# Kernel tuning notes

Hardware: AMD Instinct MI355X
Metric: run time of the kernel (lower is better)

Reference implementation:

```python
import jax, jax.numpy as jnp
import numpy as np

B, T, C = 2, 2048, 2048
N_HEADS, HEAD_DIM = 16, 128
THETA = 10000.0


def _rope_cos_sin(T, dim, theta=THETA):
    inv_freq = 1.0 / (theta ** (jnp.arange(0, dim, 2, dtype=jnp.float32) / dim))  # (dim/2,)
    t = jnp.arange(T, dtype=jnp.float32)
    freqs = jnp.outer(t, inv_freq)  # (T, dim/2)
    return jnp.cos(freqs), jnp.sin(freqs)


def _apply_rope(x, cos, sin):
    # x: (B, H, T, D); cos/sin: (T, D/2) -> broadcast over B, H
    xr = x[..., 0::2]
    xi = x[..., 1::2]
    or_ = xr * cos - xi * sin
    oi_ = xr * sin + xi * cos
    return jnp.stack([or_, oi_], axis=-1).reshape(x.shape)


def setup_inputs() -> dict:
    key = jax.random.key(0)
    ks = jax.random.split(key, 5)
    scale = 1.0 / np.sqrt(C)
    x = jax.random.normal(ks[0], (B, T, C), dtype=jnp.float32)
    wq = jax.random.normal(ks[1], (C, N_HEADS * HEAD_DIM), dtype=jnp.float32) * scale
    wk = jax.random.normal(ks[2], (C, N_HEADS * HEAD_DIM), dtype=jnp.float32) * scale
    wv = jax.random.normal(ks[3], (C, N_HEADS * HEAD_DIM), dtype=jnp.float32) * scale
    wo = jax.random.normal(ks[4], (N_HEADS * HEAD_DIM, C), dtype=jnp.float32) * scale
    mask = jnp.tril(jnp.ones((T, T), dtype=bool))[None, None]  # causal (1,1,T,T)
    return {"x": x, "mask": mask, "wq": wq, "wk": wk, "wv": wv, "wo": wo}


def reference(x, mask, wq, wk, wv, wo):
    Bx, Tx, Cx = x.shape
    cos, sin = _rope_cos_sin(Tx, HEAD_DIM)
    # projections -> (B, H, T, D)
    def proj(w):
        return (x @ w).reshape(Bx, Tx, N_HEADS, HEAD_DIM).transpose(0, 2, 1, 3)
    q = _apply_rope(proj(wq), cos, sin)
    k = _apply_rope(proj(wk), cos, sin)
    v = proj(wv)
    scores = jnp.einsum("bhqd,bhkd->bhqk", q, k) / jnp.sqrt(jnp.float32(HEAD_DIM))
    scores = jnp.where(mask, scores, -jnp.inf)
    attn = jax.nn.softmax(scores, axis=-1)
    out = jnp.einsum("bhqk,bhkd->bhqd", attn, v)
    out = out.transpose(0, 2, 1, 3).reshape(Bx, Tx, Cx)
    return out @ wo
```

## Files before the change

kernel.cpp:

```cpp
#include <hip/hip_runtime.h>
#include <stdint.h>

#define B_  2
#define T_  2048
#define C_  2048
#define NH  16
#define HD  128
#define M_  (B_*T_)

typedef unsigned short ushort_t;
typedef unsigned int uint;
typedef __attribute__((ext_vector_type(8))) short short8;
typedef __attribute__((ext_vector_type(4))) float f32x4;
typedef __attribute__((ext_vector_type(16))) float f32x16;

#if __has_builtin(__builtin_amdgcn_exp2f)
#define EXP2 __builtin_amdgcn_exp2f
#else
#define EXP2 exp2f
#endif

__device__ inline ushort_t f2b(float f) {
  union { float f; unsigned u; } x; x.f = f;
  unsigned r = (x.u + 0x7fffu + ((x.u >> 16) & 1u)) >> 16;
  return (ushort_t)r;
}
__device__ inline float b2f(ushort_t b) {
  union { unsigned u; float f; } x; x.u = ((unsigned)b) << 16;
  return x.f;
}
__device__ inline uint cvtpk(float lo, float hi) {
  uint d;
  asm("v_cvt_pk_bf16_f32 %0, %1, %2" : "=v"(d) : "v"(lo), "v"(hi));
  return d;
}
__device__ inline void pl32swap(uint& a, uint& b) {
  asm volatile("v_permlane32_swap_b32 %0, %1" : "+v"(a), "+v"(b));
}
__device__ inline void gload_lds16(const void* g, void* l) {
  __builtin_amdgcn_global_load_lds((const __attribute__((address_space(1))) void*)g,
                                   (__attribute__((address_space(3))) void*)l, 16, 0, 0);
}

__global__ __launch_bounds__(256) void cvt_f32_bf16(const float* __restrict__ in,
                                                    ushort_t* __restrict__ out, int n4) {
  int i = blockIdx.x * 256 + threadIdx.x;
  if (i >= n4) return;
  float4 v = ((const float4*)in)[i];
  unsigned long long pk = (unsigned long long)f2b(v.x)
                        | ((unsigned long long)f2b(v.y) << 16)
                        | ((unsigned long long)f2b(v.z) << 32)
                        | ((unsigned long long)f2b(v.w) << 48);
  ((unsigned long long*)out)[i] = pk;
}

template<int FROM_F32>
__global__ __launch_bounds__(256) void transpose_to_bf16(const void* __restrict__ inv,
                                                         ushort_t* __restrict__ out,
                                                         int rows, int cols) {
  __shared__ __align__(16) ushort_t tile[64][72];
  const int t = threadIdx.x;
  const int br = blockIdx.y * 64, bc = blockIdx.x * 64;
  if (FROM_F32) {
    const float* in = (const float*)inv;
    const int vc = t & 15, r0 = t >> 4;
#pragma unroll
    for (int i = 0; i < 4; i++) {
      int row = r0 + 16 * i;
      float4 v = *(const float4*)&in[(size_t)(br + row) * cols + bc + vc * 4];
      tile[row][vc * 4 + 0] = f2b(v.x);
      tile[row][vc * 4 + 1] = f2b(v.y);
      tile[row][vc * 4 + 2] = f2b(v.z);
      tile[row][vc * 4 + 3] = f2b(v.w);
    }
  } else {
    const ushort_t* in = (const ushort_t*)inv;
    const int vc = t & 7, r0 = t >> 3;
#pragma unroll
    for (int i = 0; i < 2; i++) {
      int row = r0 + 32 * i;
      short8 v = *(const short8*)&in[(size_t)(br + row) * cols + bc + vc * 8];
#pragma unroll
      for (int j = 0; j < 8; j++) tile[row][vc * 8 + j] = (ushort_t)v[j];
    }
  }
  __syncthreads();
  const int oc = t >> 2;
#pragma unroll
  for (int s2 = 0; s2 < 2; s2++) {
    int seg = (t & 3) + 4 * s2;
    short8 w;
#pragma unroll
    for (int j = 0; j < 8; j++) w[j] = (short)tile[seg * 8 + j][oc];
    *(short8*)&out[(size_t)(bc + oc) * rows + br + seg * 8] = w;
  }
}

__global__ __launch_bounds__(256) void rope_table(float* __restrict__ cs, float* __restrict__ sn) {
  int i = blockIdx.x * 256 + threadIdx.x;
  int tt = i >> 6, f = i & 63;
  float inv = powf(10000.0f, -(float)(2 * f) / 128.0f);
  float ang = (float)tt * inv;
  cs[i] = cosf(ang);
  sn[i] = sinf(ang);
}

__global__ __launch_bounds__(256) void rope_apply(ushort_t* __restrict__ Q, ushort_t* __restrict__ K,
                                                  const float* __restrict__ cs,
                                                  const float* __restrict__ sn) {
  int i = blockIdx.x * 256 + threadIdx.x;
  int row = i >> 8, g = i & 255;
  int tt = row & (T_ - 1);
  int fb = (g * 4) & 63;
  f32x4 cv = *(const f32x4*)&cs[(tt << 6) + fb];
  f32x4 sv = *(const f32x4*)&sn[(tt << 6) + fb];
  size_t idx = ((size_t)row << 11) + (size_t)g * 8;
  short8 q = *(const short8*)&Q[idx];
  short8 k = *(const short8*)&K[idx];
#pragma unroll
  for (int j = 0; j < 4; j++) {
    float c = cv[j], s = sv[j];
    float qr = b2f((ushort_t)q[2 * j]), qi = b2f((ushort_t)q[2 * j + 1]);
    q[2 * j]     = (short)f2b(qr * c - qi * s);
    q[2 * j + 1] = (short)f2b(qr * s + qi * c);
    float kr = b2f((ushort_t)k[2 * j]), ki = b2f((ushort_t)k[2 * j + 1]);
    k[2 * j]     = (short)f2b(kr * c - ki * s);
    k[2 * j + 1] = (short)f2b(kr * s + ki * c);
  }
  *(short8*)&Q[idx] = q;
  *(short8*)&K[idx] = k;
}

template<int OUTF32>
__global__ __launch_bounds__(512, 2) void gemm_bt3(const ushort_t* __restrict__ A,
                                                   const ushort_t* __restrict__ Bt0,
                                                   const ushort_t* __restrict__ Bt1,
                                                   const ushort_t* __restrict__ Bt2,
                                                   void* __restrict__ O0, void* __restrict__ O1,
                                                   void* __restrict__ O2, int N, int K) {
  extern __shared__ __align__(16) ushort_t lds[];
  const int z = blockIdx.z;
  const ushort_t* Bt = (z == 0) ? Bt0 : (z == 1) ? Bt1 : Bt2;
  void* Ov = (z == 0) ? O0 : (z == 1) ? O1 : O2;
  const int tid = threadIdx.x;
  const int lane = tid & 63, wave = tid >> 6;
  const int lr = lane & 15, lg = lane >> 4;
  const int wm = wave >> 1, wn = wave & 1;
  const int swz = lr & 7;
  const int bm = blockIdx.y, bn = blockIdx.x;
  const ushort_t* Ap = A + (size_t)bm * 256 * K;
  const ushort_t* Bp = Bt + (size_t)bn * 128 * K;
  const int NT = K >> 6;

  f32x4 acc[4][4] = {};

  auto stage = [&](int k0, int buf) {
    const int base = buf * 24576;
#pragma unroll
    for (int i = 0; i < 4; i++) {
      int idx = i * 512 + tid;
      int row = idx >> 3;
      int c = (idx & 7) ^ (row & 7);
      gload_lds16(Ap + (size_t)row * K + k0 + c * 8, &lds[(size_t)(base + idx * 8)]);
    }
#pragma unroll
    for (int i = 0; i < 2; i++) {
      int idx = i * 512 + tid;
      int row = idx >> 3;
      int c = (idx & 7) ^ (row & 7);
      gload_lds16(Bp + (size_t)row * K + k0 + c * 8, &lds[(size_t)(base + 16384 + idx * 8)]);
    }
  };

  stage(0, 0);
  stage(64, 1);

  for (int t = 0; t < NT; t++) {
    if (t + 2 < NT) stage((t + 2) << 6, (t + 2) % 3);
    if (t < NT - 2)       asm volatile("s_waitcnt vmcnt(12)" ::: "memory");
    else if (t == NT - 2) asm volatile("s_waitcnt vmcnt(6)"  ::: "memory");
    else                  asm volatile("s_waitcnt vmcnt(0)"  ::: "memory");
    __builtin_amdgcn_s_barrier();
    const int abase = (t % 3) * 24576, bbase = abase + 16384;
    __builtin_amdgcn_s_setprio(1);
#pragma unroll
    for (int kk = 0; kk < 2; kk++) {
      short8 af[4], bf[4];
      const int ch = ((kk * 4 + lg) ^ swz) * 8;
#pragma unroll
      for (int mf = 0; mf < 4; mf++)
        af[mf] = *(const short8*)&lds[abase + (wm * 64 + mf * 16 + lr) * 64 + ch];
#pragma unroll
      for (int nf = 0; nf < 4; nf++)
        bf[nf] = *(const short8*)&lds[bbase + (wn * 64 + nf * 16 + lr) * 64 + ch];
#pragma unroll
      for (int mf = 0; mf < 4; mf++)
#pragma unroll
        for (int nf = 0; nf < 4; nf++)
          acc[mf][nf] = __builtin_amdgcn_mfma_f32_16x16x32_bf16(af[mf], bf[nf], acc[mf][nf], 0, 0, 0);
    }
    __builtin_amdgcn_s_setprio(0);
    __builtin_amdgcn_s_barrier();
  }

  const int row0 = bm * 256 + wm * 64 + lg * 4;
  const int col0 = bn * 128 + wn * 64 + lr;
  if (OUTF32) {
    float* O = (float*)Ov;
#pragma unroll
    for (int mf = 0; mf < 4; mf++)
#pragma unroll
      for (int nf = 0; nf < 4; nf++)
#pragma unroll
        for (int r = 0; r < 4; r++)
          O[(size_t)(row0 + mf * 16 + r) * N + col0 + nf * 16] = acc[mf][nf][r];
  } else {
    ushort_t* O = (ushort_t*)Ov;
#pragma unroll
    for (int mf = 0; mf < 4; mf++)
#pragma unroll
      for (int nf = 0; nf < 4; nf++)
#pragma unroll
        for (int r = 0; r < 4; r++)
          O[(size_t)(row0 + mf * 16 + r) * N + col0 + nf * 16] = f2b(acc[mf][nf][r]);
  }
}

__global__ __launch_bounds__(64) void flash_attn3(const ushort_t* __restrict__ Q,
                                                  const ushort_t* __restrict__ K,
                                                  const ushort_t* __restrict__ Vt,
                                                  ushort_t* __restrict__ AO) {
  int flat = blockIdx.x;
  int swz = (flat & 7) * 128 + (flat >> 3);
  const int bh = swz >> 5, widx = swz & 31;
  const int b = bh >> 4, h = bh & 15;
  const int lane = threadIdx.x & 63;
  const int col = lane & 31, hi = lane >> 5, hioff = 4 * hi;
  const ushort_t* Qb = Q + (size_t)b * T_ * C_ + (size_t)h * HD;
  const ushort_t* Kb = K + (size_t)b * T_ * C_ + (size_t)h * HD;
  const ushort_t* Vb = Vt + (size_t)bh * (size_t)HD * T_;
  const float sc = 0.12754245f;

#pragma unroll 1
  for (int ph = 0; ph < 2; ph++) {
    const int tile = ph ? (63 - widx) : widx;
    const int q0 = tile * 32;
    const int qcol = q0 + col;
    short8 qf[8];
#pragma unroll
    for (int db = 0; db < 8; db++)
      qf[db] = *(const short8*)&Qb[(size_t)qcol * C_ + db * 16 + hi * 8];

    f32x16 o0 = {}, o1 = {}, o2 = {}, o3 = {};
    float m = -1e30f, l = 0.f;

    short8 kf[8];
#pragma unroll
    for (int db = 0; db < 8; db++)
      kf[db] = *(const short8*)&Kb[(size_t)col * C_ + db * 16 + hi * 8];

#pragma unroll 1
    for (int k0 = 0; k0 <= q0; k0 += 32) {
      f32x16 s = {};
#pragma unroll
      for (int db = 0; db < 8; db++)
        s = __builtin_amdgcn_mfma_f32_32x32x16_bf16(kf[db], qf[db], s, 0, 0, 0);
      if (k0 + 32 <= q0) {
#pragma unroll
        for (int db = 0; db < 8; db++)
          kf[db] = *(const short8*)&Kb[(size_t)(k0 + 32 + col) * C_ + db * 16 + hi * 8];
      }
      short8 va[4][2];
#pragma unroll
      for (int dblk = 0; dblk < 4; dblk++)
#pragma unroll
        for (int j = 0; j < 2; j++)
          va[dblk][j] = *(const short8*)&Vb[(size_t)(dblk * 32 + col) * T_ + k0 + j * 16 + hi * 8];

      const bool domask = (k0 + 31 > q0);
      if (domask) {
#pragma unroll
        for (int r = 0; r < 16; r++) {
          int krow = k0 + ((r & 3) + 8 * (r >> 2)) + hioff;
          float v = s[r] * sc;
          s[r] = (krow > qcol) ? -1e30f : v;
        }
      } else {
#pragma unroll
        for (int r = 0; r < 16; r++) s[r] = s[r] * sc;
      }
      float tm = s[0];
#pragma unroll
      for (int r = 1; r < 16; r++) tm = fmaxf(tm, s[r]);
      tm = fmaxf(tm, __shfl_xor(tm, 32, 64));
      if (!__all(tm <= m + 8.0f)) {
        float mn = fmaxf(m, tm);
        float corr = EXP2(m - mn);
        m = mn;
        l *= corr;
#pragma unroll
        for (int r = 0; r < 16; r++) { o0[r] *= corr; o1[r] *= corr; o2[r] *= corr; o3[r] *= corr; }
      }
#pragma unroll
      for (int r = 0; r < 16; r++) s[r] = EXP2(s[r] - m);
      float rs = s[0];
#pragma unroll
      for (int r = 1; r < 16; r++) rs += s[r];
      rs += __shfl_xor(rs, 32, 64);
      l += rs;
      uint c0 = cvtpk(s[0], s[1]),  c1 = cvtpk(s[2], s[3]);
      uint c2 = cvtpk(s[4], s[5]),  c3 = cvtpk(s[6], s[7]);
      uint c4 = cvtpk(s[8], s[9]),  c5 = cvtpk(s[10], s[11]);
      uint c6 = cvtpk(s[12], s[13]), c7 = cvtpk(s[14], s[15]);
      pl32swap(c0, c2); pl32swap(c1, c3);
      pl32swap(c4, c6); pl32swap(c5, c7);
      union { uint u[4]; short8 v; } pb0, pb1;
      pb0.u[0] = c0; pb0.u[1] = c1; pb0.u[2] = c2; pb0.u[3] = c3;
      pb1.u[0] = c4; pb1.u[1] = c5; pb1.u[2] = c6; pb1.u[3] = c7;
      o0 = __builtin_amdgcn_mfma_f32_32x32x16_bf16(va[0][0], pb0.v, o0, 0, 0, 0);
      o1 = __builtin_amdgcn_mfma_f32_32x32x16_bf16(va[1][0], pb0.v, o1, 0, 0, 0);
      o2 = __builtin_amdgcn_mfma_f32_32x32x16_bf16(va[2][0], pb0.v, o2, 0, 0, 0);
      o3 = __builtin_amdgcn_mfma_f32_32x32x16_bf16(va[3][0], pb0.v, o3, 0, 0, 0);
      o0 = __builtin_amdgcn_mfma_f32_32x32x16_bf16(va[0][1], pb1.v, o0, 0, 0, 0);
      o1 = __builtin_amdgcn_mfma_f32_32x32x16_bf16(va[1][1], pb1.v, o1, 0, 0, 0);
      o2 = __builtin_amdgcn_mfma_f32_32x32x16_bf16(va[2][1], pb1.v, o2, 0, 0, 0);
      o3 = __builtin_amdgcn_mfma_f32_32x32x16_bf16(va[3][1], pb1.v, o3, 0, 0, 0);
    }
    float inv = 1.0f / l;
    size_t rowbase = (size_t)(b * T_ + qcol) * C_ + h * HD;
#pragma unroll
    for (int r = 0; r < 16; r++) {
      int d = (r & 3) + 8 * (r >> 2) + hioff;
      AO[rowbase + d]      = f2b(o0[r] * inv);
      AO[rowbase + 32 + d] = f2b(o1[r] * inv);
      AO[rowbase + 64 + d] = f2b(o2[r] * inv);
      AO[rowbase + 96 + d] = f2b(o3[r] * inv);
    }
  }
}

extern "C" void kernel_launch(void* const* d_in, const int* in_sizes, int n_in,
                              void* d_out, int out_size, void* d_ws, size_t ws_size,
                              hipStream_t stream) {
  const float* x  = (const float*)d_in[0];
  const float* wq = (const float*)d_in[2];
  const float* wk = (const float*)d_in[3];
  const float* wv = (const float*)d_in[4];
  const float* wo = (const float*)d_in[5];

  char* ws = (char*)d_ws;
  size_t off = 0;
  auto alloc = [&](size_t bytes) { char* p = ws + off; off += (bytes + 255) & ~255ull; return p; };
  ushort_t* Qb  = (ushort_t*)alloc((size_t)M_ * C_ * 2);
  ushort_t* Kb  = (ushort_t*)alloc((size_t)M_ * C_ * 2);
  ushort_t* Vb  = (ushort_t*)alloc((size_t)M_ * C_ * 2);
  ushort_t* Vtb = (ushort_t*)alloc((size_t)M_ * C_ * 2);
  ushort_t* xb  = (ushort_t*)alloc((size_t)M_ * C_ * 2);
  ushort_t* AO  = xb;
  ushort_t* wqt = (ushort_t*)alloc((size_t)C_ * C_ * 2);
  ushort_t* wkt = (ushort_t*)alloc((size_t)C_ * C_ * 2);
  ushort_t* wvt = (ushort_t*)alloc((size_t)C_ * C_ * 2);
  ushort_t* wot = (ushort_t*)alloc((size_t)C_ * C_ * 2);
  float* cs = (float*)alloc((size_t)T_ * 64 * 4);
  float* sn = (float*)alloc((size_t)T_ * 64 * 4);

  cvt_f32_bf16<<<(M_ * C_ / 4 + 255) / 256, 256, 0, stream>>>(x, xb, M_ * C_ / 4);
  dim3 tg(C_ / 64, C_ / 64);
  transpose_to_bf16<1><<<tg, 256, 0, stream>>>(wq, wqt, C_, C_);
  transpose_to_bf16<1><<<tg, 256, 0, stream>>>(wk, wkt, C_, C_);
  transpose_to_bf16<1><<<tg, 256, 0, stream>>>(wv, wvt, C_, C_);
  transpose_to_bf16<1><<<tg, 256, 0, stream>>>(wo, wot, C_, C_);
  rope_table<<<T_ * 64 / 256, 256, 0, stream>>>(cs, sn);
  gemm_bt3<0><<<dim3(C_ / 128, M_ / 256, 3), 512, 147456, stream>>>(
      xb, wqt, wkt, wvt, Qb, Kb, Vb, C_, C_);
  rope_apply<<<M_ * C_ / 8 / 256, 256, 0, stream>>>(Qb, Kb, cs, sn);
  for (int b = 0; b < B_; b++)
    transpose_to_bf16<0><<<dim3(T_ / 64, T_ / 64), 256, 0, stream>>>(
        Vb + (size_t)b * T_ * C_, Vtb + (size_t)b * T_ * C_, T_, C_);
  flash_attn3<<<dim3(B_ * NH * 32), 64, 0, stream>>>(Qb, Kb, Vtb, AO);
  gemm_bt3<1><<<dim3(C_ / 128, M_ / 256, 1), 512, 147456, stream>>>(
      AO, wot, wot, wot, d_out, d_out, d_out, C_, C_);
  (void)in_sizes; (void)n_in; (void)out_size; (void)ws_size;
}
```

Before: 456.7 us.

## Split causal KV loop across two waves per block with LDS merge

```diff
diff --git a/kernel.cpp b/kernel.cpp
--- a/kernel.cpp
+++ b/kernel.cpp
@@ -226,14 +226,17 @@
   }
 }
 
-__global__ __launch_bounds__(64) void flash_attn3(const ushort_t* __restrict__ Q,
-                                                  const ushort_t* __restrict__ K,
-                                                  const ushort_t* __restrict__ Vt,
-                                                  ushort_t* __restrict__ AO) {
+__global__ __launch_bounds__(128) void flash_attn4(const ushort_t* __restrict__ Q,
+                                                   const ushort_t* __restrict__ K,
+                                                   const ushort_t* __restrict__ Vt,
+                                                   ushort_t* __restrict__ AO) {
+  __shared__ float oLds[2][64][64];
+  __shared__ float mlLds[2][2][32];
   int flat = blockIdx.x;
   int swz = (flat & 7) * 128 + (flat >> 3);
   const int bh = swz >> 5, widx = swz & 31;
   const int b = bh >> 4, h = bh & 15;
+  const int w = threadIdx.x >> 6;
   const int lane = threadIdx.x & 63;
   const int col = lane & 31, hi = lane >> 5, hioff = 4 * hi;
   const ushort_t* Qb = Q + (size_t)b * T_ * C_ + (size_t)h * HD;
@@ -253,89 +256,109 @@
 
     f32x16 o0 = {}, o1 = {}, o2 = {}, o3 = {};
     float m = -1e30f, l = 0.f;
-
-    short8 kf[8];
-#pragma unroll
-    for (int db = 0; db < 8; db++)
-      kf[db] = *(const short8*)&Kb[(size_t)col * C_ + db * 16 + hi * 8];
+    const int kstart = w * 32;
+
+    if (kstart <= q0) {
+      short8 kf[8];
+#pragma unroll
+      for (int db = 0; db < 8; db++)
+        kf[db] = *(const short8*)&Kb[(size_t)(kstart + col) * C_ + db * 16 + hi * 8];
 
 #pragma unroll 1
-    for (int k0 = 0; k0 <= q0; k0 += 32) {
-      f32x16 s = {};
-#pragma unroll
-      for (int db = 0; db < 8; db++)
-        s = __builtin_amdgcn_mfma_f32_32x32x16_bf16(kf[db], qf[db], s, 0, 0, 0);
-      if (k0 + 32 <= q0) {
-#pragma unroll
-        for (int db = 0; db < 8; db++)
-          kf[db] = *(const short8*)&Kb[(size_t)(k0 + 32 + col) * C_ + db * 16 + hi * 8];
+      for (int k0 = kstart; k0 <= q0; k0 += 64) {
+        f32x16 sa = {}, sb = {};
+#pragma unroll
+        for (int db = 0; db < 4; db++) {
+          sa = __builtin_amdgcn_mfma_f32_32x32x16_bf16(kf[db],     qf[db],     sa, 0, 0, 0);
+          sb = __builtin_amdgcn_mfma_f32_32x32x16_bf16(kf[db + 4], qf[db + 4], sb, 0, 0, 0);
+        }
+        if (k0 + 64 <= q0) {
+#pragma unroll
+          for (int db = 0; db < 8; db++)
+            kf[db] = *(const short8*)&Kb[(size_t)(k0 + 64 + col) * C_ + db * 16 + hi * 8];
+        }
+        short8 va[4][2];
+#pragma unroll
+        for (int dblk = 0; dblk < 4; dblk++)
+#pragma unroll
+          for (int j = 0; j < 2; j++)
+            va[dblk][j] = *(const short8*)&Vb[(size_t)(dblk * 32 + col) * T_ + k0 + j * 16 + hi * 8];
+
+        f32x16 s;
+        const bool domask = (k0 + 31 > q0);
+        if (domask) {
+#pragma unroll
+          for (int r = 0; r < 16; r++) {
+            int krow = k0 + ((r & 3) + 8 * (r >> 2)) + hioff;
+            float v = (sa[r] + sb[r]) * sc;
+            s[r] = (krow > qcol) ? -1e30f : v;
+          }
+        } else {
+#pragma unroll
+          for (int r = 0; r < 16; r++) s[r] = (sa[r] + sb[r]) * sc;
+        }
+        float tm = s[0];
+#pragma unroll
+        for (int r = 1; r < 16; r++) tm = fmaxf(tm, s[r]);
+        tm = fmaxf(tm, __shfl_xor(tm, 32, 64));
+        if (!__all(tm <= m + 8.0f)) {
+          float mn = fmaxf(m, tm);
+          float corr = EXP2(m - mn);
+          m = mn;
+          l *= corr;
+#pragma unroll
+          for (int r = 0; r < 16; r++) { o0[r] *= corr; o1[r] *= corr; o2[r] *= corr; o3[r] *= corr; }
+        }
+#pragma unroll
+        for (int r = 0; r < 16; r++) s[r] = EXP2(s[r] - m);
+        float rs = s[0];
+#pragma unroll
+        for (int r = 1; r < 16; r++) rs += s[r];
+        rs += __shfl_xor(rs, 32, 64);
+        l += rs;
+        uint c0 = cvtpk(s[0], s[1]),  c1 = cvtpk(s[2], s[3]);
+        uint c2 = cvtpk(s[4], s[5]),  c3 = cvtpk(s[6], s[7]);
+        uint c4 = cvtpk(s[8], s[9]),  c5 = cvtpk(s[10], s[11]);
+        uint c6 = cvtpk(s[12], s[13]), c7 = cvtpk(s[14], s[15]);
+        pl32swap(c0, c2); pl32swap(c1, c3);
+        pl32swap(c4, c6); pl32swap(c5, c7);
+        union { uint u[4]; short8 v; } pb0, pb1;
+        pb0.u[0] = c0; pb0.u[1] = c1; pb0.u[2] = c2; pb0.u[3] = c3;
+        pb1.u[0] = c4; pb1.u[1] = c5; pb1.u[2] = c6; pb1.u[3] = c7;
+        o0 = __builtin_amdgcn_mfma_f32_32x32x16_bf16(va[0][0], pb0.v, o0, 0, 0, 0);
+        o1 = __builtin_amdgcn_mfma_f32_32x32x16_bf16(va[1][0], pb0.v, o1, 0, 0, 0);
+        o2 = __builtin_amdgcn_mfma_f32_32x32x16_bf16(va[2][0], pb0.v, o2, 0, 0, 0);
+        o3 = __builtin_amdgcn_mfma_f32_32x32x16_bf16(va[3][0], pb0.v, o3, 0, 0, 0);
+        o0 = __builtin_amdgcn_mfma_f32_32x32x16_bf16(va[0][1], pb1.v, o0, 0, 0, 0);
+        o1 = __builtin_amdgcn_mfma_f32_32x32x16_bf16(va[1][1], pb1.v, o1, 0, 0, 0);
+        o2 = __builtin_amdgcn_mfma_f32_32x32x16_bf16(va[2][1], pb1.v, o2, 0, 0, 0);
+        o3 = __builtin_amdgcn_mfma_f32_32x32x16_bf16(va[3][1], pb1.v, o3, 0, 0, 0);
       }
-      short8 va[4][2];
-#pragma unroll
-      for (int dblk = 0; dblk < 4; dblk++)
-#pragma unroll
-        for (int j = 0; j < 2; j++)
-          va[dblk][j] = *(const short8*)&Vb[(size_t)(dblk * 32 + col) * T_ + k0 + j * 16 + hi * 8];
-
-      const bool domask = (k0 + 31 > q0);
-      if (domask) {
-#pragma unroll
-        for (int r = 0; r < 16; r++) {
-          int krow = k0 + ((r & 3) + 8 * (r >> 2)) + hioff;
-          float v = s[r] * sc;
-          s[r] = (krow > qcol) ? -1e30f : v;
-        }
-      } else {
-#pragma unroll
-        for (int r = 0; r < 16; r++) s[r] = s[r] * sc;
-      }
-      float tm = s[0];
-#pragma unroll
-      for (int r = 1; r < 16; r++) tm = fmaxf(tm, s[r]);
-      tm = fmaxf(tm, __shfl_xor(tm, 32, 64));
-      if (!__all(tm <= m + 8.0f)) {
-        float mn = fmaxf(m, tm);
-        float corr = EXP2(m - mn);
-        m = mn;
-        l *= corr;
-#pragma unroll
-        for (int r = 0; r < 16; r++) { o0[r] *= corr; o1[r] *= corr; o2[r] *= corr; o3[r] *= corr; }
-      }
-#pragma unroll
-      for (int r = 0; r < 16; r++) s[r] = EXP2(s[r] - m);
-      float rs = s[0];
-#pragma unroll
-      for (int r = 1; r < 16; r++) rs += s[r];
-      rs += __shfl_xor(rs, 32, 64);
-      l += rs;
-      uint c0 = cvtpk(s[0], s[1]),  c1 = cvtpk(s[2], s[3]);
-      uint c2 = cvtpk(s[4], s[5]),  c3 = cvtpk(s[6], s[7]);
-      uint c4 = cvtpk(s[8], s[9]),  c5 = cvtpk(s[10], s[11]);
-      uint c6 = cvtpk(s[12], s[13]), c7 = cvtpk(s[14], s[15]);
-      pl32swap(c0, c2); pl32swap(c1, c3);
-      pl32swap(c4, c6); pl32swap(c5, c7);
-      union { uint u[4]; short8 v; } pb0, pb1;
-      pb0.u[0] = c0; pb0.u[1] = c1; pb0.u[2] = c2; pb0.u[3] = c3;
-      pb1.u[0] = c4; pb1.u[1] = c5; pb1.u[2] = c6; pb1.u[3] = c7;
-      o0 = __builtin_amdgcn_mfma_f32_32x32x16_bf16(va[0][0], pb0.v, o0, 0, 0, 0);
-      o1 = __builtin_amdgcn_mfma_f32_32x32x16_bf16(va[1][0], pb0.v, o1, 0, 0, 0);
-      o2 = __builtin_amdgcn_mfma_f32_32x32x16_bf16(va[2][0], pb0.v, o2, 0, 0, 0);
-      o3 = __builtin_amdgcn_mfma_f32_32x32x16_bf16(va[3][0], pb0.v, o3, 0, 0, 0);
-      o0 = __builtin_amdgcn_mfma_f32_32x32x16_bf16(va[0][1], pb1.v, o0, 0, 0, 0);
-      o1 = __builtin_amdgcn_mfma_f32_32x32x16_bf16(va[1][1], pb1.v, o1, 0, 0, 0);
-      o2 = __builtin_amdgcn_mfma_f32_32x32x16_bf16(va[2][1], pb1.v, o2, 0, 0, 0);
-      o3 = __builtin_amdgcn_mfma_f32_32x32x16_bf16(va[3][1], pb1.v, o3, 0, 0, 0);
-    }
-    float inv = 1.0f / l;
+    }
+#pragma unroll
+    for (int r = 0; r < 16; r++) {
+      oLds[w][r][lane]      = o0[r];
+      oLds[w][16 + r][lane] = o1[r];
+      oLds[w][32 + r][lane] = o2[r];
+      oLds[w][48 + r][lane] = o3[r];
+    }
+    if (lane < 32) { mlLds[w][0][lane] = m; mlLds[w][1][lane] = l; }
+    __syncthreads();
+    float m0 = mlLds[0][0][col], m1 = mlLds[1][0][col];
+    float M = fmaxf(m0, m1);
+    float s0 = EXP2(m0 - M), s1 = EXP2(m1 - M);
+    float L = mlLds[0][1][col] * s0 + mlLds[1][1][col] * s1;
+    float inv = 1.0f / L;
     size_t rowbase = (size_t)(b * T_ + qcol) * C_ + h * HD;
 #pragma unroll
-    for (int r = 0; r < 16; r++) {
+    for (int j = 0; j < 32; j++) {
+      int R = w * 32 + j;
+      float merged = (oLds[0][R][lane] * s0 + oLds[1][R][lane] * s1) * inv;
+      int db = R >> 4, r = R & 15;
       int d = (r & 3) + 8 * (r >> 2) + hioff;
-      AO[rowbase + d]      = f2b(o0[r] * inv);
-      AO[rowbase + 32 + d] = f2b(o1[r] * inv);
-      AO[rowbase + 64 + d] = f2b(o2[r] * inv);
-      AO[rowbase + 96 + d] = f2b(o3[r] * inv);
-    }
+      AO[rowbase + db * 32 + d] = f2b(merged);
+    }
+    __syncthreads();
   }
 }
 
@@ -377,7 +400,7 @@
   for (int b = 0; b < B_; b++)
     transpose_to_bf16<0><<<dim3(T_ / 64, T_ / 64), 256, 0, stream>>>(
         Vb + (size_t)b * T_ * C_, Vtb + (size_t)b * T_ * C_, T_, C_);
-  flash_attn3<<<dim3(B_ * NH * 32), 64, 0, stream>>>(Qb, Kb, Vtb, AO);
+  flash_attn4<<<dim3(B_ * NH * 32), 128, 0, stream>>>(Qb, Kb, Vtb, AO);
   gemm_bt3<1><<<dim3(C_ / 128, M_ / 256, 1), 512, 147456, stream>>>(
       AO, wot, wot, wot, d_out, d_out, d_out, C_, C_);
   (void)in_sizes; (void)n_in; (void)out_size; (void)ws_size;
```

Measured after the change: 463.6 us. No clear change (+1.5%).
